# Performance work log

Hardware: AMD Instinct MI355X
Metric: run time of the kernel (lower is better)

## Reference

```python
import jax, jax.numpy as jnp
import numpy as np

DROP_P = 0.1
REG = 0.01

NU, NI, D, B = 12000, 16000, 64, 1024


def setup_inputs() -> dict:
    key = jax.random.key(0)
    ks = jax.random.split(key, 10)
    return {
        "L_u": jax.random.normal(ks[0], (NU, NU), dtype=jnp.float32),
        "L_i": jax.random.normal(ks[1], (NI, NI), dtype=jnp.float32),
        "user_embed": jax.random.normal(ks[2], (NU, D), dtype=jnp.float32),
        "item_embed": jax.random.normal(ks[3], (NI, D), dtype=jnp.float32),
        "mask_u": jax.random.uniform(ks[4], (B, NU), dtype=jnp.float32),
        "mask_p": jax.random.uniform(ks[5], (B, NI), dtype=jnp.float32),
        "mask_n": jax.random.uniform(ks[6], (B, NI), dtype=jnp.float32),
        "user": jax.random.randint(ks[7], (B,), 0, NU),
        "pos_item": jax.random.randint(ks[8], (B,), 0, NI),
        "nega_item": jax.random.randint(ks[9], (B,), 0, NI),
    }


def reference(L_u, L_i, user_embed, item_embed, mask_u, mask_p, mask_n, user, pos_item, nega_item):
    # torch Dropout scales by 1/(1-p); code multiplies back by (1-p) -> net binary mask.
    keep_u = (mask_u >= DROP_P).astype(L_u.dtype)
    keep_p = (mask_p >= DROP_P).astype(L_i.dtype)
    keep_n = (mask_n >= DROP_P).astype(L_i.dtype)

    # gather filter rows, mask, project through embedding table: [B, N] @ [N, D]
    final_user = (L_u[user] * keep_u) @ user_embed        # [B, D]
    final_pos = (L_i[pos_item] * keep_p) @ item_embed    # [B, D]
    final_nega = (L_i[nega_item] * keep_n) @ item_embed  # [B, D]

    res_nega = jnp.sum(final_user * final_nega, axis=1)  # [B]
    nega_weight = jax.lax.stop_gradient(
        1.0 - jnp.log10(1.0 - jnp.minimum(jax.nn.sigmoid(res_nega), 0.99))
    )
    out = jax.nn.sigmoid(jnp.sum(final_user * final_pos, axis=1) - nega_weight * res_nega)

    reg_term = REG * (jnp.sum(final_user ** 2) + jnp.sum(final_pos ** 2) + jnp.sum(final_nega ** 2))
    batch = user.shape[0]
    return (-jnp.sum(jnp.log(out)) + reg_term) / batch
```

## Files before the change

### kernel.cpp

```cpp
#include <hip/hip_runtime.h>
#include <math.h>

#define NU_ 12000
#define NI_ 16000
#define NPU 12288
#define NPI 16384
#define DD 64
#define BB 1024
#define KC 512

typedef unsigned short ushort_t;
typedef __bf16 bf16x8 __attribute__((ext_vector_type(8)));
typedef float  f32x4  __attribute__((ext_vector_type(4)));
typedef unsigned short ushort4v __attribute__((ext_vector_type(4)));

static __device__ __forceinline__ ushort_t f2bf(float f) {
    __bf16 h = (__bf16)f;
    return __builtin_bit_cast(unsigned short, h);
}

__global__ __launch_bounds__(256) void gde_transpose(
    const float* __restrict__ E, ushort_t* __restrict__ Et, int N, int Np)
{
    __shared__ ushort_t Ls[64][65];
    const int n0  = blockIdx.x * 64;
    const int tid = threadIdx.x;
    const int dg  = tid & 15;
    const int nr  = tid >> 4;
#pragma unroll
    for (int nn = 0; nn < 4; ++nn) {
        const int nl = nn * 16 + nr;
        const int n  = n0 + nl;
        float4 v = make_float4(0.f, 0.f, 0.f, 0.f);
        if (n < N) v = *(const float4*)(E + (size_t)n * DD + dg * 4);
        Ls[nl][dg * 4 + 0] = f2bf(v.x);
        Ls[nl][dg * 4 + 1] = f2bf(v.y);
        Ls[nl][dg * 4 + 2] = f2bf(v.z);
        Ls[nl][dg * 4 + 3] = f2bf(v.w);
    }
    __syncthreads();
    const int d   = tid & 63;
    const int nl0 = (tid >> 6) * 16;
#pragma unroll
    for (int g = 0; g < 4; ++g) {
        ushort4v t;
#pragma unroll
        for (int i = 0; i < 4; ++i) t[i] = Ls[nl0 + g * 4 + i][d];
        *(ushort4v*)(Et + (size_t)d * Np + n0 + nl0 + g * 4) = t;
    }
}

__global__ __launch_bounds__(256, 3) void gde_gemm(
    const float* __restrict__ L_u, const float* __restrict__ L_i,
    const ushort_t* __restrict__ EtU, const ushort_t* __restrict__ EtI,
    const float* __restrict__ mu,  const float* __restrict__ mp,
    const float* __restrict__ mn,
    const int* __restrict__ user, const int* __restrict__ pos,
    const int* __restrict__ nega,
    float* __restrict__ P, int S)
{
    __shared__ ushort_t As[32 * 512];

    const int rt  = blockIdx.x;
    const int s   = blockIdx.y;
    const int j   = blockIdx.z;
    const int tid = threadIdx.x;
    const int w   = tid >> 6;
    const int l   = tid & 63;

    const float* L; const ushort_t* Et; const float* M; const int* idx;
    int N, Np;
    if (j == 0)      { L = L_u; Et = EtU; M = mu; idx = user; N = NU_; Np = NPU; }
    else if (j == 1) { L = L_i; Et = EtI; M = mp; idx = pos;  N = NI_; Np = NPI; }
    else             { L = L_i; Et = EtI; M = mn; idx = nega; N = NI_; Np = NPI; }

    const int base = rt * 32;
    const float* Lr[8];
    const float* Mr[8];
#pragma unroll
    for (int r = 0; r < 8; ++r) {
        const int row = base + w * 8 + r;
        Lr[r] = L + (size_t)idx[row] * N;
        Mr[r] = M + (size_t)row * N;
    }

    const int dcol = l & 15;
    const ushort_t* Eb[4];
#pragma unroll
    for (int df = 0; df < 4; ++df)
        Eb[df] = Et + (size_t)(df * 16 + dcol) * Np;

    f32x4 acc[8];
#pragma unroll
    for (int i = 0; i < 8; ++i) acc[i] = (f32x4){0.f, 0.f, 0.f, 0.f};

    const int nc  = (N + KC - 1) / KC;
    const int kb0 = (s * nc) / S;
    const int kb1 = ((s + 1) * nc) / S;

    for (int kb = kb0; kb < kb1; ++kb) {
        const int k0 = kb * KC;
        const int kg = k0 + 8 * l;
        const bool valid = (kg < N);

#pragma unroll
        for (int g = 0; g < 2; ++g) {
            float4 a0[4], a1[4], m0[4], m1[4];
#pragma unroll
            for (int r = 0; r < 4; ++r) {
                const int rr = g * 4 + r;
                if (valid) {
                    a0[r] = *(const float4*)(Lr[rr] + kg);
                    a1[r] = *(const float4*)(Lr[rr] + kg + 4);
                    m0[r] = *(const float4*)(Mr[rr] + kg);
                    m1[r] = *(const float4*)(Mr[rr] + kg + 4);
                } else {
                    a0[r] = a1[r] = m0[r] = m1[r] = make_float4(0.f,0.f,0.f,0.f);
                }
            }
#pragma unroll
            for (int r = 0; r < 4; ++r) {
                bf16x8 af;
                af[0] = (__bf16)((m0[r].x >= 0.1f) ? a0[r].x : 0.0f);
                af[1] = (__bf16)((m0[r].y >= 0.1f) ? a0[r].y : 0.0f);
                af[2] = (__bf16)((m0[r].z >= 0.1f) ? a0[r].z : 0.0f);
                af[3] = (__bf16)((m0[r].w >= 0.1f) ? a0[r].w : 0.0f);
                af[4] = (__bf16)((m1[r].x >= 0.1f) ? a1[r].x : 0.0f);
                af[5] = (__bf16)((m1[r].y >= 0.1f) ? a1[r].y : 0.0f);
                af[6] = (__bf16)((m1[r].z >= 0.1f) ? a1[r].z : 0.0f);
                af[7] = (__bf16)((m1[r].w >= 0.1f) ? a1[r].w : 0.0f);
                const int rowl = w * 8 + g * 4 + r;
                *(bf16x8*)((char*)As + rowl * 1024 +
                           ((l * 16) ^ ((rowl & 7) << 4))) = af;
            }
        }
        __syncthreads();

#pragma unroll
        for (int t4 = 0; t4 < 4; ++t4) {
            const int ks   = w * 4 + t4;
            const int colb = ks * 64 + 16 * (l >> 4);
            const int r0 = dcol, r1 = 16 + dcol;
            const bf16x8 af0 = *(const bf16x8*)((char*)As + r0 * 1024 +
                                                (colb ^ ((r0 & 7) << 4)));
            const bf16x8 af1 = *(const bf16x8*)((char*)As + r1 * 1024 +
                                                (colb ^ ((r1 & 7) << 4)));
            const int kk = k0 + ks * 32 + 8 * (l >> 4);
            const bf16x8 b0 = *(const bf16x8*)(Eb[0] + kk);
            const bf16x8 b1 = *(const bf16x8*)(Eb[1] + kk);
            const bf16x8 b2 = *(const bf16x8*)(Eb[2] + kk);
            const bf16x8 b3 = *(const bf16x8*)(Eb[3] + kk);
            acc[0] = __builtin_amdgcn_mfma_f32_16x16x32_bf16(af0, b0, acc[0], 0, 0, 0);
            acc[1] = __builtin_amdgcn_mfma_f32_16x16x32_bf16(af0, b1, acc[1], 0, 0, 0);
            acc[2] = __builtin_amdgcn_mfma_f32_16x16x32_bf16(af0, b2, acc[2], 0, 0, 0);
            acc[3] = __builtin_amdgcn_mfma_f32_16x16x32_bf16(af0, b3, acc[3], 0, 0, 0);
            acc[4] = __builtin_amdgcn_mfma_f32_16x16x32_bf16(af1, b0, acc[4], 0, 0, 0);
            acc[5] = __builtin_amdgcn_mfma_f32_16x16x32_bf16(af1, b1, acc[5], 0, 0, 0);
            acc[6] = __builtin_amdgcn_mfma_f32_16x16x32_bf16(af1, b2, acc[6], 0, 0, 0);
            acc[7] = __builtin_amdgcn_mfma_f32_16x16x32_bf16(af1, b3, acc[7], 0, 0, 0);
        }
        __syncthreads();
    }

    float* Pb = P + ((size_t)(j * (S * 4) + s * 4 + w) * BB + base) * DD;
#pragma unroll
    for (int ri = 0; ri < 4; ++ri) {
        const int m = (l >> 4) * 4 + ri;
        Pb[(size_t)m * DD +  0 + dcol] = acc[0][ri];
        Pb[(size_t)m * DD + 16 + dcol] = acc[1][ri];
        Pb[(size_t)m * DD + 32 + dcol] = acc[2][ri];
        Pb[(size_t)m * DD + 48 + dcol] = acc[3][ri];
        Pb[(size_t)(m + 16) * DD +  0 + dcol] = acc[4][ri];
        Pb[(size_t)(m + 16) * DD + 16 + dcol] = acc[5][ri];
        Pb[(size_t)(m + 16) * DD + 32 + dcol] = acc[6][ri];
        Pb[(size_t)(m + 16) * DD + 48 + dcol] = acc[7][ri];
    }
}

__global__ __launch_bounds__(256) void gde_finalize(
    const float* __restrict__ P, int Seff,
    float* __restrict__ term, float* __restrict__ regp)
{
    const int b    = blockIdx.x * 4 + (threadIdx.x >> 6);
    const int lane = threadIdx.x & 63;
    const size_t joff = (size_t)Seff * BB * DD;

    float fu = 0.f, fp_ = 0.f, fn = 0.f;
    for (int s = 0; s < Seff; ++s) {
        const size_t base = ((size_t)s * BB + b) * DD + lane;
        fu  += P[base];
        fp_ += P[base + joff];
        fn  += P[base + 2 * joff];
    }

    float rp = fu * fp_;
    float rn = fu * fn;
    float rg = fu * fu + fp_ * fp_ + fn * fn;
#pragma unroll
    for (int o = 32; o > 0; o >>= 1) {
        rp += __shfl_xor(rp, o);
        rn += __shfl_xor(rn, o);
        rg += __shfl_xor(rg, o);
    }

    if (lane == 0) {
        const float sn = 1.0f / (1.0f + expf(-rn));
        const float w  = 1.0f - log10f(1.0f - fminf(sn, 0.99f));
        const float x  = rp - w * rn;
        const float t  = -x;
        term[b] = fmaxf(t, 0.0f) + log1pf(expf(-fabsf(t)));
        regp[b] = rg;
    }
}

__global__ __launch_bounds__(256) void gde_reduce(
    const float* __restrict__ term, const float* __restrict__ regp,
    float* __restrict__ out)
{
    __shared__ float sm[256];
    const int t = threadIdx.x;
    float v = 0.f;
    for (int i = t; i < BB; i += 256)
        v += term[i] + 0.01f * regp[i];
    sm[t] = v;
    __syncthreads();
    for (int o = 128; o > 0; o >>= 1) {
        if (t < o) sm[t] += sm[t + o];
        __syncthreads();
    }
    if (t == 0) out[0] = sm[0] / (float)BB;
}

extern "C" void kernel_launch(void* const* d_in, const int* in_sizes, int n_in,
                              void* d_out, int out_size, void* d_ws, size_t ws_size,
                              hipStream_t stream)
{
    const float* L_u = (const float*)d_in[0];
    const float* L_i = (const float*)d_in[1];
    const float* ue  = (const float*)d_in[2];
    const float* ie  = (const float*)d_in[3];
    const float* mu  = (const float*)d_in[4];
    const float* mp  = (const float*)d_in[5];
    const float* mn  = (const float*)d_in[6];
    const int* user  = (const int*)d_in[7];
    const int* pos   = (const int*)d_in[8];
    const int* nega  = (const int*)d_in[9];
    float* out = (float*)d_out;

    const size_t etU_b  = (size_t)DD * NPU * 2;
    const size_t etI_b  = (size_t)DD * NPI * 2;
    const size_t slice  = (size_t)3 * BB * DD * 4;
    const size_t fixed  = etU_b + etI_b + 2 * BB * 4 + 256;
    int S = 8;
    while (S > 1 && (size_t)(4 * S) * slice + fixed > ws_size) --S;
    const int Seff = 4 * S;

    float*    P    = (float*)d_ws;
    ushort_t* EtU  = (ushort_t*)((char*)d_ws + (size_t)Seff * slice);
    ushort_t* EtI  = (ushort_t*)((char*)EtU + etU_b);
    float*    term = (float*)((char*)EtI + etI_b);
    float*    regp = term + BB;

    gde_transpose<<<dim3(NPU / 64), dim3(256), 0, stream>>>(ue, EtU, NU_, NPU);
    gde_transpose<<<dim3(NPI / 64), dim3(256), 0, stream>>>(ie, EtI, NI_, NPI);

    gde_gemm<<<dim3(32, S, 3), dim3(256), 0, stream>>>(
        L_u, L_i, EtU, EtI, mu, mp, mn, user, pos, nega, P, S);

    gde_finalize<<<dim3(BB / 4), dim3(256), 0, stream>>>(P, Seff, term, regp);
    gde_reduce<<<dim3(1), dim3(256), 0, stream>>>(term, regp, out);
}
```

Measured before the change: 108.7 us.

## Register-prefetch next K chunk of masked rows and halve chunk size

Restructures the split-K GEMM loop so the fp32 filter rows and dropout masks for the next 256-wide K chunk are loaded into registers while the current chunk is converted, stored to LDS and consumed by MFMAs. The embedding B-fragments are loaded before the barrier, and 32-bit byte offsets replace per-row pointers to save registers. KC drops from 512 to 256 and occupancy hint from 3 to 2 blocks per CU. The goal is to hide global load latency behind compute, at the cost of more live registers and more loop iterations with barriers.

```diff
diff --git a/kernel.cpp b/kernel.cpp
--- a/kernel.cpp
+++ b/kernel.cpp
@@ -7,7 +7,8 @@
 #define NPI 16384
 #define DD 64
 #define BB 1024
-#define KC 512
+#define KC 256
+#define SPL 8
 
 typedef unsigned short ushort_t;
 typedef __bf16 bf16x8 __attribute__((ext_vector_type(8)));
@@ -50,7 +51,7 @@
     }
 }
 
-__global__ __launch_bounds__(256, 3) void gde_gemm(
+__global__ __launch_bounds__(256, 2) void gde_gemm(
     const float* __restrict__ L_u, const float* __restrict__ L_i,
     const ushort_t* __restrict__ EtU, const ushort_t* __restrict__ EtI,
     const float* __restrict__ mu,  const float* __restrict__ mp,
@@ -59,7 +60,7 @@
     const int* __restrict__ nega,
     float* __restrict__ P, int S)
 {
-    __shared__ ushort_t As[32 * 512];
+    __shared__ ushort_t As[32 * 256];
 
     const int rt  = blockIdx.x;
     const int s   = blockIdx.y;
@@ -75,20 +76,19 @@
     else             { L = L_i; Et = EtI; M = mn; idx = nega; N = NI_; Np = NPI; }
 
     const int base = rt * 32;
-    const float* Lr[8];
-    const float* Mr[8];
+    unsigned int Loff[8], Moff[8];
 #pragma unroll
     for (int r = 0; r < 8; ++r) {
         const int row = base + w * 8 + r;
-        Lr[r] = L + (size_t)idx[row] * N;
-        Mr[r] = M + (size_t)row * N;
+        Loff[r] = (unsigned int)idx[row] * (unsigned int)(N * 4);
+        Moff[r] = (unsigned int)row * (unsigned int)(N * 4);
     }
 
     const int dcol = l & 15;
+    const int g4   = l >> 4;
     const ushort_t* Eb[4];
 #pragma unroll
-    for (int df = 0; df < 4; ++df)
-        Eb[df] = Et + (size_t)(df * 16 + dcol) * Np;
+    for (int df = 0; df < 4; ++df) Eb[df] = Et + (size_t)(df * 16 + dcol) * Np;
 
     f32x4 acc[8];
 #pragma unroll
@@ -98,74 +98,86 @@
     const int kb0 = (s * nc) / S;
     const int kb1 = ((s + 1) * nc) / S;
 
+    float4 La[8], Ma[8];
+#pragma unroll
+    for (int r = 0; r < 8; ++r) { La[r] = make_float4(0.f,0.f,0.f,0.f); Ma[r] = La[r]; }
+
+    {
+        const int kg = kb0 * KC + 4 * l;
+        const size_t boff = (size_t)kg * 4u;
+        if (kg < N) {
+#pragma unroll
+            for (int r = 0; r < 8; ++r) {
+                La[r] = *(const float4*)((const char*)L + Loff[r] + boff);
+                Ma[r] = *(const float4*)((const char*)M + Moff[r] + boff);
+            }
+        }
+    }
+
     for (int kb = kb0; kb < kb1; ++kb) {
-        const int k0 = kb * KC;
-        const int kg = k0 + 8 * l;
-        const bool valid = (kg < N);
-
-#pragma unroll
-        for (int g = 0; g < 2; ++g) {
-            float4 a0[4], a1[4], m0[4], m1[4];
-#pragma unroll
-            for (int r = 0; r < 4; ++r) {
-                const int rr = g * 4 + r;
-                if (valid) {
-                    a0[r] = *(const float4*)(Lr[rr] + kg);
-                    a1[r] = *(const float4*)(Lr[rr] + kg + 4);
-                    m0[r] = *(const float4*)(Mr[rr] + kg);
-                    m1[r] = *(const float4*)(Mr[rr] + kg + 4);
-                } else {
-                    a0[r] = a1[r] = m0[r] = m1[r] = make_float4(0.f,0.f,0.f,0.f);
+#pragma unroll
+        for (int r = 0; r < 8; ++r) {
+            const int row = w * 8 + r;
+            ushort4v t;
+            t[0] = (Ma[r].x >= 0.1f) ? f2bf(La[r].x) : (ushort_t)0;
+            t[1] = (Ma[r].y >= 0.1f) ? f2bf(La[r].y) : (ushort_t)0;
+            t[2] = (Ma[r].z >= 0.1f) ? f2bf(La[r].z) : (ushort_t)0;
+            t[3] = (Ma[r].w >= 0.1f) ? f2bf(La[r].w) : (ushort_t)0;
+            *(ushort4v*)((char*)As + (row << 9) + ((l * 8) ^ ((row & 7) << 4))) = t;
+        }
+
+        bf16x8 bfr[2][4];
+#pragma unroll
+        for (int h = 0; h < 2; ++h) {
+            const int kk = kb * KC + (2 * w + h) * 32 + 8 * g4;
+#pragma unroll
+            for (int df = 0; df < 4; ++df)
+                bfr[h][df] = *(const bf16x8*)(Eb[df] + kk);
+        }
+        asm volatile("" ::: "memory");
+
+        if (kb + 1 < kb1) {
+            const int kg = (kb + 1) * KC + 4 * l;
+            const size_t boff = (size_t)kg * 4u;
+            if (kg < N) {
+#pragma unroll
+                for (int r = 0; r < 8; ++r) {
+                    La[r] = *(const float4*)((const char*)L + Loff[r] + boff);
+                    Ma[r] = *(const float4*)((const char*)M + Moff[r] + boff);
                 }
             }
-#pragma unroll
-            for (int r = 0; r < 4; ++r) {
-                bf16x8 af;
-                af[0] = (__bf16)((m0[r].x >= 0.1f) ? a0[r].x : 0.0f);
-                af[1] = (__bf16)((m0[r].y >= 0.1f) ? a0[r].y : 0.0f);
-                af[2] = (__bf16)((m0[r].z >= 0.1f) ? a0[r].z : 0.0f);
-                af[3] = (__bf16)((m0[r].w >= 0.1f) ? a0[r].w : 0.0f);
-                af[4] = (__bf16)((m1[r].x >= 0.1f) ? a1[r].x : 0.0f);
-                af[5] = (__bf16)((m1[r].y >= 0.1f) ? a1[r].y : 0.0f);
-                af[6] = (__bf16)((m1[r].z >= 0.1f) ? a1[r].z : 0.0f);
-                af[7] = (__bf16)((m1[r].w >= 0.1f) ? a1[r].w : 0.0f);
-                const int rowl = w * 8 + g * 4 + r;
-                *(bf16x8*)((char*)As + rowl * 1024 +
-                           ((l * 16) ^ ((rowl & 7) << 4))) = af;
-            }
-        }
-        __syncthreads();
-
-#pragma unroll
-        for (int t4 = 0; t4 < 4; ++t4) {
-            const int ks   = w * 4 + t4;
-            const int colb = ks * 64 + 16 * (l >> 4);
+        }
+
+        asm volatile("s_waitcnt lgkmcnt(0)" ::: "memory");
+        __builtin_amdgcn_s_barrier();
+        asm volatile("" ::: "memory");
+
+#pragma unroll
+        for (int h = 0; h < 2; ++h) {
+            const int ks = 2 * w + h;
+            const int cb = 64 * ks + 16 * g4;
             const int r0 = dcol, r1 = 16 + dcol;
-            const bf16x8 af0 = *(const bf16x8*)((char*)As + r0 * 1024 +
-                                                (colb ^ ((r0 & 7) << 4)));
-            const bf16x8 af1 = *(const bf16x8*)((char*)As + r1 * 1024 +
-                                                (colb ^ ((r1 & 7) << 4)));
-            const int kk = k0 + ks * 32 + 8 * (l >> 4);
-            const bf16x8 b0 = *(const bf16x8*)(Eb[0] + kk);
-            const bf16x8 b1 = *(const bf16x8*)(Eb[1] + kk);
-            const bf16x8 b2 = *(const bf16x8*)(Eb[2] + kk);
-            const bf16x8 b3 = *(const bf16x8*)(Eb[3] + kk);
-            acc[0] = __builtin_amdgcn_mfma_f32_16x16x32_bf16(af0, b0, acc[0], 0, 0, 0);
-            acc[1] = __builtin_amdgcn_mfma_f32_16x16x32_bf16(af0, b1, acc[1], 0, 0, 0);
-            acc[2] = __builtin_amdgcn_mfma_f32_16x16x32_bf16(af0, b2, acc[2], 0, 0, 0);
-            acc[3] = __builtin_amdgcn_mfma_f32_16x16x32_bf16(af0, b3, acc[3], 0, 0, 0);
-            acc[4] = __builtin_amdgcn_mfma_f32_16x16x32_bf16(af1, b0, acc[4], 0, 0, 0);
-            acc[5] = __builtin_amdgcn_mfma_f32_16x16x32_bf16(af1, b1, acc[5], 0, 0, 0);
-            acc[6] = __builtin_amdgcn_mfma_f32_16x16x32_bf16(af1, b2, acc[6], 0, 0, 0);
-            acc[7] = __builtin_amdgcn_mfma_f32_16x16x32_bf16(af1, b3, acc[7], 0, 0, 0);
-        }
-        __syncthreads();
+            const bf16x8 af0 = *(const bf16x8*)((char*)As + (r0 << 9) + (cb ^ ((r0 & 7) << 4)));
+            const bf16x8 af1 = *(const bf16x8*)((char*)As + (r1 << 9) + (cb ^ ((r1 & 7) << 4)));
+            acc[0] = __builtin_amdgcn_mfma_f32_16x16x32_bf16(af0, bfr[h][0], acc[0], 0, 0, 0);
+            acc[1] = __builtin_amdgcn_mfma_f32_16x16x32_bf16(af0, bfr[h][1], acc[1], 0, 0, 0);
+            acc[2] = __builtin_amdgcn_mfma_f32_16x16x32_bf16(af0, bfr[h][2], acc[2], 0, 0, 0);
+            acc[3] = __builtin_amdgcn_mfma_f32_16x16x32_bf16(af0, bfr[h][3], acc[3], 0, 0, 0);
+            acc[4] = __builtin_amdgcn_mfma_f32_16x16x32_bf16(af1, bfr[h][0], acc[4], 0, 0, 0);
+            acc[5] = __builtin_amdgcn_mfma_f32_16x16x32_bf16(af1, bfr[h][1], acc[5], 0, 0, 0);
+            acc[6] = __builtin_amdgcn_mfma_f32_16x16x32_bf16(af1, bfr[h][2], acc[6], 0, 0, 0);
+            acc[7] = __builtin_amdgcn_mfma_f32_16x16x32_bf16(af1, bfr[h][3], acc[7], 0, 0, 0);
+        }
+
+        asm volatile("" ::: "memory");
+        __builtin_amdgcn_s_barrier();
+        asm volatile("" ::: "memory");
     }
 
     float* Pb = P + ((size_t)(j * (S * 4) + s * 4 + w) * BB + base) * DD;
 #pragma unroll
     for (int ri = 0; ri < 4; ++ri) {
-        const int m = (l >> 4) * 4 + ri;
+        const int m = g4 * 4 + ri;
         Pb[(size_t)m * DD +  0 + dcol] = acc[0][ri];
         Pb[(size_t)m * DD + 16 + dcol] = acc[1][ri];
         Pb[(size_t)m * DD + 32 + dcol] = acc[2][ri];
@@ -251,7 +263,7 @@
     const size_t etI_b  = (size_t)DD * NPI * 2;
     const size_t slice  = (size_t)3 * BB * DD * 4;
     const size_t fixed  = etU_b + etI_b + 2 * BB * 4 + 256;
-    int S = 8;
+    int S = SPL;
     while (S > 1 && (size_t)(4 * S) * slice + fixed > ws_size) --S;
     const int Seff = 4 * S;
 
```

Result: faster. 102.1 us (-6.1%).
